# Kernel optimization log

Hardware: AMD Instinct MI355X
Metric: run time of the kernel (lower is better)

The kernel has to match this reference:

```python
import jax, jax.numpy as jnp
import numpy as np

B, T, D = 4, 2048, 128

def setup_inputs() -> dict:
    key = jax.random.key(0)
    k1, k2, k3 = jax.random.split(key, 3)
    x = jax.random.normal(k1, (B, T, D), dtype=jnp.float32)
    # torch nn.Linear default init ~ U(-1/sqrt(D), 1/sqrt(D))
    lim = 1.0 / np.sqrt(D)
    W = jax.random.uniform(k2, (3 * D, D), dtype=jnp.float32, minval=-lim, maxval=lim)
    b = jax.random.uniform(k3, (3 * D,), dtype=jnp.float32, minval=-lim, maxval=lim)
    return {"x": x, "W": W, "b": b}

def reference(x, W, b):
    Bx, Tx, Dx = x.shape
    qkv = (x @ W.T + b).reshape(Bx, Tx, 3, Dx)
    q, k, v = qkv[:, :, 0], qkv[:, :, 1], qkv[:, :, 2]
    # positive feature map: elu(x) + 1
    q = jax.nn.elu(q) + 1.0
    k = jax.nn.elu(k) + 1.0
    # causal linear attention via outer-product cumsum (same math as torch module)
    kv = jnp.einsum('bti,btj->btij', k, v)      # (B,T,D,D)
    kv_cum = jnp.cumsum(kv, axis=1)             # prefix sums of k v^T
    k_cum = jnp.cumsum(k, axis=1)               # prefix sums of k
    num = jnp.einsum('bti,btij->btj', q, kv_cum)
    den = jnp.einsum('bti,bti->bt', q, k_cum)[..., None] + 1e-6
    return num / den
```

## Files before the change

kernel.cpp:

```cpp
#include <hip/hip_runtime.h>
#include <math.h>

#define NCn 64
#define NCHUNK 256
#define NROW 8192

__device__ __forceinline__ float elu1(float v) {
    return (v > 0.f) ? v + 1.f : expf(v);
}

__global__ __launch_bounds__(256) void wt_kernel(
    const float* __restrict__ W, float* __restrict__ Wt)
{
    __shared__ float t[32][33];
    const int bi = blockIdx.x >> 2;
    const int bj = blockIdx.x & 3;
    const int r0 = bi * 32, c0 = bj * 32;
    const int tr = threadIdx.x >> 5, tc = threadIdx.x & 31;
#pragma unroll
    for (int rr = tr; rr < 32; rr += 8)
        t[rr][tc] = W[(r0 + rr) * 128 + c0 + tc];
    __syncthreads();
#pragma unroll
    for (int rr = tr; rr < 32; rr += 8)
        Wt[(c0 + rr) * 384 + r0 + tc] = t[tc][rr];
}

__global__ __launch_bounds__(192) void qkv_kernel(
    const float* __restrict__ x, const float* __restrict__ Wt,
    const float* __restrict__ bias, float* __restrict__ qb,
    float* __restrict__ kb, float* __restrict__ vb)
{
    __shared__ __align__(16) float xs[16 * 128];
    const int tid = threadIdx.x;
    const int row0 = blockIdx.x * 16;

    {
        const float4* xg = (const float4*)(x + (size_t)row0 * 128);
        float4* xls = (float4*)xs;
        for (int i = tid; i < 16 * 32; i += 192) xls[i] = xg[i];
    }
    __syncthreads();

    const int c0 = tid, c1 = tid + 192;
    float acc0[16], acc1[16];
#pragma unroll
    for (int r = 0; r < 16; ++r) { acc0[r] = 0.f; acc1[r] = 0.f; }

    for (int k4 = 0; k4 < 32; ++k4) {
        float w0[4], w1[4];
#pragma unroll
        for (int u = 0; u < 4; ++u) {
            w0[u] = Wt[(size_t)(k4 * 4 + u) * 384 + c0];
            w1[u] = Wt[(size_t)(k4 * 4 + u) * 384 + c1];
        }
        float4 xv[16];
#pragma unroll
        for (int r = 0; r < 16; ++r) xv[r] = *(const float4*)&xs[r * 128 + k4 * 4];
#pragma unroll
        for (int r = 0; r < 16; ++r) {
            acc0[r] += xv[r].x * w0[0] + xv[r].y * w0[1] + xv[r].z * w0[2] + xv[r].w * w0[3];
            acc1[r] += xv[r].x * w1[0] + xv[r].y * w1[1] + xv[r].z * w1[2] + xv[r].w * w1[3];
        }
    }

    const float bb0 = bias[c0], bb1 = bias[c1];
#pragma unroll
    for (int r = 0; r < 16; ++r) {
        const size_t row = (size_t)(row0 + r);
        float v0 = acc0[r] + bb0;
        float v1 = acc1[r] + bb1;
        if (c0 < 128) qb[row * 128 + c0] = elu1(v0);
        else          kb[row * 128 + (c0 - 128)] = elu1(v0);
        if (c1 < 256) kb[row * 128 + (c1 - 128)] = elu1(v1);
        else          vb[row * 128 + (c1 - 256)] = v1;
    }
}

__global__ __launch_bounds__(256) void cs_kernel(
    const float* __restrict__ qb, const float* __restrict__ kb,
    const float* __restrict__ vb,
    float* __restrict__ kvb, float* __restrict__ ksb,
    float* __restrict__ scb, float* __restrict__ rsb)
{
    __shared__ __align__(16) float smem[9600];
    const int tid = threadIdx.x;
    const int b = blockIdx.x;

    if (b < 512) {
        const int cb = b >> 1, jh = b & 1;
        float* sK  = smem;
        float* sVh = smem + 4224;
        {
            const float4* kg = (const float4*)(kb + (size_t)cb * 4096);
#pragma unroll
            for (int i = 0; i < 4; ++i) {
                int idx = tid + i * 256;
                int r = idx >> 5, c4 = idx & 31;
                *(float4*)&sK[r * 132 + c4 * 4] = kg[idx];
            }
            const float* vg = vb + (size_t)cb * 4096 + jh * 64;
#pragma unroll
            for (int i = 0; i < 2; ++i) {
                int idx = tid + i * 256;
                int r = idx >> 4, c4 = idx & 15;
                *(float4*)&sVh[r * 68 + c4 * 4] = *(const float4*)(vg + r * 128 + c4 * 4);
            }
        }
        __syncthreads();

        const int i0 = (tid >> 4) * 8;
        const int j0 = (tid & 15) * 4;
        float acc[8][4];
#pragma unroll
        for (int a = 0; a < 8; ++a)
#pragma unroll
            for (int c = 0; c < 4; ++c) acc[a][c] = 0.f;

#pragma unroll 2
        for (int t = 0; t < 32; ++t) {
            float4 ka  = *(const float4*)&sK[t * 132 + i0];
            float4 kb4 = *(const float4*)&sK[t * 132 + i0 + 4];
            float4 vv  = *(const float4*)&sVh[t * 68 + j0];
            float kk[8] = {ka.x, ka.y, ka.z, ka.w, kb4.x, kb4.y, kb4.z, kb4.w};
#pragma unroll
            for (int a = 0; a < 8; ++a) {
                acc[a][0] += kk[a] * vv.x;
                acc[a][1] += kk[a] * vv.y;
                acc[a][2] += kk[a] * vv.z;
                acc[a][3] += kk[a] * vv.w;
            }
        }
        float* outp = kvb + (size_t)cb * 16384 + jh * 64;
#pragma unroll
        for (int a = 0; a < 8; ++a)
            *(float4*)&outp[(i0 + a) * 128 + j0] =
                make_float4(acc[a][0], acc[a][1], acc[a][2], acc[a][3]);
    } else {
        const int cb = b - 512;
        float* sQ  = smem;
        float* sK2 = smem + 4224;
        float* sSc = smem + 8448;
        {
            const float4* qg = (const float4*)(qb + (size_t)cb * 4096);
            const float4* kg = (const float4*)(kb + (size_t)cb * 4096);
#pragma unroll
            for (int i = 0; i < 4; ++i) {
                int idx = tid + i * 256;
                int r = idx >> 5, c4 = idx & 31;
                *(float4*)&sQ[r * 132 + c4 * 4]  = qg[idx];
                *(float4*)&sK2[r * 132 + c4 * 4] = kg[idx];
            }
        }
        __syncthreads();

        const int ta  = tid >> 3;
        const int tp0 = (tid & 7) * 4;
        float d[4] = {0.f, 0.f, 0.f, 0.f};
#pragma unroll 4
        for (int k4 = 0; k4 < 32; ++k4) {
            float4 qa = *(const float4*)&sQ[ta * 132 + k4 * 4];
#pragma unroll
            for (int u = 0; u < 4; ++u) {
                float4 kv = *(const float4*)&sK2[(tp0 + u) * 132 + k4 * 4];
                d[u] += qa.x * kv.x + qa.y * kv.y + qa.z * kv.z + qa.w * kv.w;
            }
        }
        float4 m;
        m.x = (tp0 + 0 <= ta) ? d[0] : 0.f;
        m.y = (tp0 + 1 <= ta) ? d[1] : 0.f;
        m.z = (tp0 + 2 <= ta) ? d[2] : 0.f;
        m.w = (tp0 + 3 <= ta) ? d[3] : 0.f;
        *(float4*)&sSc[ta * 36 + tp0] = m;
        *(float4*)(scb + (size_t)cb * 1024 + ta * 32 + tp0) = m;
        __syncthreads();

        if (tid < 32) {
            float s = 0.f;
#pragma unroll
            for (int tp = 0; tp < 32; ++tp) s += sSc[tid * 36 + tp];
            rsb[cb * 32 + tid] = s;
        } else if (tid >= 64 && tid < 192) {
            const int i = tid - 64;
            float s = 0.f;
#pragma unroll
            for (int t = 0; t < 32; ++t) s += sK2[t * 132 + i];
            ksb[cb * 128 + i] = s;
        }
    }
}

__global__ __launch_bounds__(256) void prefix_kernel(
    float* __restrict__ kvb, float* __restrict__ ksb)
{
    const int tid = threadIdx.x;
    if (blockIdx.x < 256) {
        const int L = blockIdx.x * 256 + tid;
        const int b = L >> 14, ij = L & 16383;
        float* p = kvb + (size_t)b * NCn * 16384 + ij;
        float run = 0.f;
        for (int g = 0; g < 4; ++g) {
            float buf[16];
#pragma unroll
            for (int j = 0; j < 16; ++j) buf[j] = p[(size_t)(g * 16 + j) * 16384];
#pragma unroll
            for (int j = 0; j < 16; ++j) {
                p[(size_t)(g * 16 + j) * 16384] = run;
                run += buf[j];
            }
        }
    } else {
        const int L = (blockIdx.x - 256) * 256 + tid;
        const int b = L >> 7, i = L & 127;
        float* p = ksb + (size_t)b * NCn * 128 + i;
        float run = 0.f;
        for (int g = 0; g < 4; ++g) {
            float buf[16];
#pragma unroll
            for (int j = 0; j < 16; ++j) buf[j] = p[(size_t)(g * 16 + j) * 128];
#pragma unroll
            for (int j = 0; j < 16; ++j) {
                p[(size_t)(g * 16 + j) * 128] = run;
                run += buf[j];
            }
        }
    }
}

__global__ __launch_bounds__(256) void out_kernel(
    const float* __restrict__ qb, const float* __restrict__ vb,
    const float* __restrict__ kvb, const float* __restrict__ ksb,
    const float* __restrict__ scb, const float* __restrict__ rsb,
    float* __restrict__ out)
{
    __shared__ __align__(16) float sQ[32 * 132];
    __shared__ __align__(16) float sVs[32 * 36];
    __shared__ __align__(16) float sSc[32 * 36];
    __shared__ __align__(16) float sKp[128];
    __shared__ float sDen[32];

    const int tid = threadIdx.x;
    const int cb = blockIdx.x >> 2;
    const int ch = blockIdx.x & 3;

    {
        const float4* qg = (const float4*)(qb + (size_t)cb * 4096);
#pragma unroll
        for (int i = 0; i < 4; ++i) {
            int idx = tid + i * 256;
            int r = idx >> 5, c4 = idx & 31;
            *(float4*)&sQ[r * 132 + c4 * 4] = qg[idx];
        }
        {
            int r = tid >> 3, c4 = tid & 7;
            *(float4*)&sVs[r * 36 + c4 * 4] =
                *(const float4*)(vb + (size_t)cb * 4096 + r * 128 + ch * 32 + c4 * 4);
            *(float4*)&sSc[r * 36 + c4 * 4] =
                *(const float4*)(scb + (size_t)cb * 1024 + tid * 4);
        }
        if (tid < 128) sKp[tid] = ksb[cb * 128 + tid];
    }
    __syncthreads();

    if (tid < 32) {
        float d = 0.f;
#pragma unroll
        for (int k4 = 0; k4 < 32; ++k4) {
            float4 a  = *(const float4*)&sQ[tid * 132 + k4 * 4];
            float4 b2 = *(const float4*)&sKp[k4 * 4];
            d += a.x * b2.x + a.y * b2.y + a.z * b2.z + a.w * b2.w;
        }
        sDen[tid] = d + rsb[cb * 32 + tid] + 1e-6f;
    }

    const int row = tid >> 3;
    const int c4  = tid & 7;
    const float* Sg = kvb + (size_t)cb * 16384 + ch * 32 + c4 * 4;

    float a0 = 0.f, a1 = 0.f, a2 = 0.f, a3 = 0.f;
#pragma unroll 8
    for (int k = 0; k < 128; ++k) {
        const float qv = sQ[row * 132 + k];
        float4 s = *(const float4*)(Sg + (size_t)k * 128);
        a0 += qv * s.x; a1 += qv * s.y; a2 += qv * s.z; a3 += qv * s.w;
    }
#pragma unroll 8
    for (int tp = 0; tp < 32; ++tp) {
        const float sc = sSc[row * 36 + tp];
        float4 v = *(const float4*)&sVs[tp * 36 + c4 * 4];
        a0 += sc * v.x; a1 += sc * v.y; a2 += sc * v.z; a3 += sc * v.w;
    }
    __syncthreads();

    const float dv = sDen[row];
    *(float4*)(out + ((size_t)cb * 32 + row) * 128 + ch * 32 + c4 * 4) =
        make_float4(a0 / dv, a1 / dv, a2 / dv, a3 / dv);
}

extern "C" void kernel_launch(void* const* d_in, const int* in_sizes, int n_in,
                              void* d_out, int out_size, void* d_ws, size_t ws_size,
                              hipStream_t stream)
{
    const float* x    = (const float*)d_in[0];
    const float* W    = (const float*)d_in[1];
    const float* bias = (const float*)d_in[2];
    float* out = (float*)d_out;

    float* ws  = (float*)d_ws;
    float* qb  = ws;
    float* kb  = ws + 1048576;
    float* vb  = ws + 2097152;
    float* kvb = ws + 3145728;
    float* ksb = ws + 7340032;
    float* scb = ws + 7372800;
    float* rsb = ws + 7634944;
    float* Wt  = ws + 7643136;

    wt_kernel<<<48, 256, 0, stream>>>(W, Wt);
    qkv_kernel<<<NROW / 16, 192, 0, stream>>>(x, Wt, bias, qb, kb, vb);
    cs_kernel<<<768, 256, 0, stream>>>(qb, kb, vb, kvb, ksb, scb, rsb);
    prefix_kernel<<<258, 256, 0, stream>>>(kvb, ksb);
    out_kernel<<<1024, 256, 0, stream>>>(qb, vb, kvb, ksb, scb, rsb, out);
}
```

Baseline: 133.3 us.

## Replace QKV projection with 2D shared-memory tiled GEMM and drop transpose kernel

```diff
diff --git a/kernel.cpp b/kernel.cpp
--- a/kernel.cpp
+++ b/kernel.cpp
@@ -9,71 +9,77 @@
     return (v > 0.f) ? v + 1.f : expf(v);
 }
 
-__global__ __launch_bounds__(256) void wt_kernel(
-    const float* __restrict__ W, float* __restrict__ Wt)
-{
-    __shared__ float t[32][33];
-    const int bi = blockIdx.x >> 2;
-    const int bj = blockIdx.x & 3;
-    const int r0 = bi * 32, c0 = bj * 32;
-    const int tr = threadIdx.x >> 5, tc = threadIdx.x & 31;
-#pragma unroll
-    for (int rr = tr; rr < 32; rr += 8)
-        t[rr][tc] = W[(r0 + rr) * 128 + c0 + tc];
-    __syncthreads();
-#pragma unroll
-    for (int rr = tr; rr < 32; rr += 8)
-        Wt[(c0 + rr) * 384 + r0 + tc] = t[tc][rr];
-}
-
-__global__ __launch_bounds__(192) void qkv_kernel(
-    const float* __restrict__ x, const float* __restrict__ Wt,
-    const float* __restrict__ bias, float* __restrict__ qb,
-    float* __restrict__ kb, float* __restrict__ vb)
-{
-    __shared__ __align__(16) float xs[16 * 128];
+__global__ __launch_bounds__(256) void qkv_kernel(
+    const float* __restrict__ x, const float* __restrict__ W,
+    const float* __restrict__ bias,
+    float* __restrict__ qb, float* __restrict__ kb, float* __restrict__ vb)
+{
+    __shared__ __align__(16) float sX[64 * 36];
+    __shared__ __align__(16) float sW[64 * 36];
     const int tid = threadIdx.x;
-    const int row0 = blockIdx.x * 16;
-
-    {
-        const float4* xg = (const float4*)(x + (size_t)row0 * 128);
-        float4* xls = (float4*)xs;
-        for (int i = tid; i < 16 * 32; i += 192) xls[i] = xg[i];
-    }
-    __syncthreads();
-
-    const int c0 = tid, c1 = tid + 192;
-    float acc0[16], acc1[16];
-#pragma unroll
-    for (int r = 0; r < 16; ++r) { acc0[r] = 0.f; acc1[r] = 0.f; }
-
-    for (int k4 = 0; k4 < 32; ++k4) {
-        float w0[4], w1[4];
-#pragma unroll
-        for (int u = 0; u < 4; ++u) {
-            w0[u] = Wt[(size_t)(k4 * 4 + u) * 384 + c0];
-            w1[u] = Wt[(size_t)(k4 * 4 + u) * 384 + c1];
-        }
-        float4 xv[16];
-#pragma unroll
-        for (int r = 0; r < 16; ++r) xv[r] = *(const float4*)&xs[r * 128 + k4 * 4];
-#pragma unroll
-        for (int r = 0; r < 16; ++r) {
-            acc0[r] += xv[r].x * w0[0] + xv[r].y * w0[1] + xv[r].z * w0[2] + xv[r].w * w0[3];
-            acc1[r] += xv[r].x * w1[0] + xv[r].y * w1[1] + xv[r].z * w1[2] + xv[r].w * w1[3];
-        }
-    }
-
-    const float bb0 = bias[c0], bb1 = bias[c1];
-#pragma unroll
-    for (int r = 0; r < 16; ++r) {
-        const size_t row = (size_t)(row0 + r);
-        float v0 = acc0[r] + bb0;
-        float v1 = acc1[r] + bb1;
-        if (c0 < 128) qb[row * 128 + c0] = elu1(v0);
-        else          kb[row * 128 + (c0 - 128)] = elu1(v0);
-        if (c1 < 256) kb[row * 128 + (c1 - 128)] = elu1(v1);
-        else          vb[row * 128 + (c1 - 256)] = v1;
+    const int m0 = blockIdx.x * 64;
+    const int cbase = blockIdx.y * 64;
+
+    const int ty = tid >> 4, tx = tid & 15;
+    const int r0 = ty * 4;
+
+    float acc[4][4];
+#pragma unroll
+    for (int r = 0; r < 4; ++r)
+#pragma unroll
+        for (int c = 0; c < 4; ++c) acc[r][c] = 0.f;
+
+    for (int kc = 0; kc < 4; ++kc) {
+        __syncthreads();
+        {
+            int idx = tid;
+#pragma unroll
+            for (int i = 0; i < 2; ++i, idx += 256) {
+                const int row = idx >> 3, f = idx & 7;
+                *(float4*)&sX[row * 36 + f * 4] =
+                    *(const float4*)(x + (size_t)(m0 + row) * 128 + kc * 32 + f * 4);
+                *(float4*)&sW[row * 36 + f * 4] =
+                    *(const float4*)(W + (size_t)(cbase + row) * 128 + kc * 32 + f * 4);
+            }
+        }
+        __syncthreads();
+
+#pragma unroll
+        for (int k4 = 0; k4 < 8; ++k4) {
+            float4 xr[4], wr[4];
+#pragma unroll
+            for (int r = 0; r < 4; ++r)
+                xr[r] = *(const float4*)&sX[(r0 + r) * 36 + k4 * 4];
+#pragma unroll
+            for (int c = 0; c < 4; ++c)
+                wr[c] = *(const float4*)&sW[(tx + 16 * c) * 36 + k4 * 4];
+#pragma unroll
+            for (int r = 0; r < 4; ++r)
+#pragma unroll
+                for (int c = 0; c < 4; ++c)
+                    acc[r][c] += xr[r].x * wr[c].x + xr[r].y * wr[c].y
+                               + xr[r].z * wr[c].z + xr[r].w * wr[c].w;
+        }
+    }
+
+    float* dst; int coff; bool act;
+    if (cbase < 128)      { dst = qb; coff = cbase;       act = true;  }
+    else if (cbase < 256) { dst = kb; coff = cbase - 128; act = true;  }
+    else                  { dst = vb; coff = cbase - 256; act = false; }
+
+    float bb[4];
+#pragma unroll
+    for (int c = 0; c < 4; ++c) bb[c] = bias[cbase + tx + 16 * c];
+
+#pragma unroll
+    for (int r = 0; r < 4; ++r) {
+        float* drow = dst + (size_t)(m0 + r0 + r) * 128 + coff + tx;
+#pragma unroll
+        for (int c = 0; c < 4; ++c) {
+            float o = acc[r][c] + bb[c];
+            if (act) o = elu1(o);
+            drow[16 * c] = o;
+        }
     }
 }
 
@@ -314,10 +320,8 @@
     float* ksb = ws + 7340032;
     float* scb = ws + 7372800;
     float* rsb = ws + 7634944;
-    float* Wt  = ws + 7643136;
-
-    wt_kernel<<<48, 256, 0, stream>>>(W, Wt);
-    qkv_kernel<<<NROW / 16, 192, 0, stream>>>(x, Wt, bias, qb, kb, vb);
+
+    qkv_kernel<<<dim3(128, 6), 256, 0, stream>>>(x, W, bias, qb, kb, vb);
     cs_kernel<<<768, 256, 0, stream>>>(qb, kb, vb, kvb, ksb, scb, rsb);
     prefix_kernel<<<258, 256, 0, stream>>>(kvb, ksb);
     out_kernel<<<1024, 256, 0, stream>>>(qb, vb, kvb, ksb, scb, rsb, out);
```

Result: faster. 121.3 us (-9.0%).
